# Performance work log

Measured on AMD Instinct MI355X. Metric: run time of the kernel, lower is better.

## Reference

```python
import jax, jax.numpy as jnp
import numpy as np

B, S, H, V = 64, 512, 1024, 32000


def setup_inputs() -> dict:
    key = jax.random.key(0)
    ks = jax.random.split(key, 20)
    sd = 0.02
    inp = {
        'x': jax.random.randint(ks[0], (B, 1), 0, V),
        'h_prev': jax.random.normal(ks[1], (B, H), dtype=jnp.float32),
        'annotations': jax.random.normal(ks[2], (B, S, H), dtype=jnp.float32),
        # embedding table
        'emb': jax.random.normal(ks[3], (V, H), dtype=jnp.float32) * sd,
        # attention MLP: Linear(2H -> H), ReLU, Linear(H -> 1)
        'attn_W1': jax.random.normal(ks[4], (H, 2 * H), dtype=jnp.float32) * sd,
        'attn_b1': jnp.zeros((H,), jnp.float32),
        'attn_W2': jax.random.normal(ks[5], (1, H), dtype=jnp.float32) * sd,
        'attn_b2': jnp.zeros((1,), jnp.float32),
        # GRU cell linears (input_size = 2H). NOTE: original code has a bug where
        # weights_hr is never used (r uses weights_hz); we replicate that, so no Whr.
        'W_ir': jax.random.normal(ks[6], (H, 2 * H), dtype=jnp.float32) * sd,
        'b_ir': jnp.zeros((H,), jnp.float32),
        'W_iz': jax.random.normal(ks[7], (H, 2 * H), dtype=jnp.float32) * sd,
        'b_iz': jnp.zeros((H,), jnp.float32),
        'W_in': jax.random.normal(ks[8], (H, 2 * H), dtype=jnp.float32) * sd,
        'b_in': jnp.zeros((H,), jnp.float32),
        'W_hz': jax.random.normal(ks[9], (H, H), dtype=jnp.float32) * sd,
        'b_hz': jnp.zeros((H,), jnp.float32),
        'W_hn': jax.random.normal(ks[10], (H, H), dtype=jnp.float32) * sd,
        'b_hn': jnp.zeros((H,), jnp.float32),
        # output projection H -> V
        'W_out': jax.random.normal(ks[11], (V, H), dtype=jnp.float32) * sd,
        'b_out': jnp.zeros((V,), jnp.float32),
    }
    return inp


def _lin(x, W, b):
    # torch nn.Linear: y = x @ W.T + b, W has shape (out, in)
    return x @ W.T + b


def reference(x, h_prev, annotations, emb, attn_W1, attn_b1, attn_W2, attn_b2,
              W_ir, b_ir, W_iz, b_iz, W_in, b_in, W_hz, b_hz, W_hn, b_hn,
              W_out, b_out):
    # embedding lookup, squeeze time dim: (B, H)
    embed = emb[x[:, 0]]

    # additive attention: concat(annotations, expanded hidden) -> MLP -> softmax
    # split W1 over the concat axis to avoid materializing the [B,S,2H] concat:
    # concat @ W1.T == annotations @ W1[:, :H].T + hidden @ W1[:, H:].T
    hA = jnp.einsum('bsh,kh->bsk', annotations, attn_W1[:, :H])  # (B,S,H)
    hB = h_prev @ attn_W1[:, H:].T                               # (B,H)
    hidden_act = jax.nn.relu(hA + hB[:, None, :] + attn_b1)
    scores = jnp.einsum('bsk,k->bs', hidden_act, attn_W2[0]) + attn_b2[0]
    attention_weights = jax.nn.softmax(scores, axis=1)[:, :, None]  # (B,S,1)

    # context vector
    context = jnp.sum(attention_weights * annotations, axis=1)  # (B,H)
    xc = jnp.concatenate([context, embed], axis=1)              # (B,2H)

    # GRU cell (faithful to the original, including the weights_hz reuse in r)
    hz = _lin(h_prev, W_hz, b_hz)
    z = jax.nn.sigmoid(_lin(xc, W_iz, b_iz) + hz)
    r = jax.nn.sigmoid(_lin(xc, W_ir, b_ir) + hz)  # bug replicated: uses W_hz
    g = jnp.tanh(_lin(xc, W_in, b_in) + r * _lin(h_prev, W_hn, b_hn))
    h_new = (1.0 - z) * g + z * h_prev

    output = _lin(h_new, W_out, b_out)  # (B,V)
    return output, h_new, attention_weights
```

## Files before the change

kernel.cpp:

```cpp
#include <hip/hip_runtime.h>


typedef __bf16 bf16;
typedef __attribute__((ext_vector_type(4))) float  f32x4;
typedef __attribute__((ext_vector_type(4))) float  fx4;
typedef __attribute__((ext_vector_type(8))) bf16   bf16x8;
typedef __attribute__((ext_vector_type(4))) bf16   bf16x4;
typedef __attribute__((ext_vector_type(4))) unsigned int u32x4;
typedef __attribute__((ext_vector_type(2))) unsigned int u32x2;

#define MFMA16x16x32(a, b, c) __builtin_amdgcn_mfma_f32_16x16x32_bf16(a, b, c, 0, 0, 0)

#define Bb   64
#define Ss   512
#define Hh   1024
#define Vv   32000
#define Mtot (Bb * Ss)

#define WS_HPREV_B   0
#define WS_HNEW_B    131072
#define WS_XC_B      262144
#define WS_W1A_B     524288
#define WS_P_HB      2621440
#define WS_P_HZ      3670016
#define WS_P_HN      4718592
#define WS_P_IZ      5767168
#define WS_P_IR      6815744
#define WS_P_IN      7864320
#define WS_SCORES    8912896
#define WS_CTX       11010048
#define WS_ANNB      13107200

#define OUT_LOGITS   0
#define OUT_HNEW     2048000
#define OUT_AW       2113536

__device__ __forceinline__ float bf2f(unsigned short u) {
    unsigned int x = ((unsigned int)u) << 16;
    float f;
    __builtin_memcpy(&f, &x, 4);
    return f;
}

__device__ __forceinline__ void gload_lds16(const bf16* g, bf16* l)
{
    __builtin_amdgcn_global_load_lds(
        (const __attribute__((address_space(1))) unsigned int*)g,
        (__attribute__((address_space(3))) unsigned int*)l,
        16, 0, 0);
}

__global__ void k_prep(const int* __restrict__ x, const float* __restrict__ h_prev,
                       const float* __restrict__ emb, const float* __restrict__ attn_W1,
                       bf16* __restrict__ h_prev_b, bf16* __restrict__ xc_b,
                       bf16* __restrict__ W1a_b)
{
    int bid = blockIdx.x, t = threadIdx.x;
    if (bid < 64) {
        int b = bid;
        int row = x[b];
        for (int i = t; i < Hh; i += 256) {
            h_prev_b[b * Hh + i]          = (bf16)h_prev[b * Hh + i];
            xc_b[b * 2048 + Hh + i]       = (bf16)emb[(size_t)row * Hh + i];
        }
    } else {
        int row = bid - 64;
        int k4 = t * 4;
        fx4 v = *(const fx4*)(attn_W1 + (size_t)row * 2048 + k4);
        bf16x4 o;
#pragma unroll
        for (int q = 0; q < 4; q++) o[q] = (bf16)v[q];
        *(bf16x4*)(W1a_b + (size_t)row * Hh + k4) = o;
    }
}

__global__ void k_convann(const float* __restrict__ ann, bf16* __restrict__ annb)
{
    size_t i = ((size_t)blockIdx.x * 256 + threadIdx.x) * 8;
    size_t stride = (size_t)gridDim.x * 256 * 8;
    size_t n = (size_t)Mtot * Hh;
    for (; i < n; i += stride) {
        fx4 v0 = *(const fx4*)(ann + i);
        fx4 v1 = *(const fx4*)(ann + i + 4);
        bf16x8 o;
#pragma unroll
        for (int q = 0; q < 4; q++) { o[q] = (bf16)v0[q]; o[q + 4] = (bf16)v1[q]; }
        *(bf16x8*)(annb + i) = o;
    }
}

__global__ __launch_bounds__(256, 2) void k_sgemm(
    const bf16* __restrict__ A, int lda, int kchunk,
    const float* __restrict__ B0, const float* __restrict__ B1, const float* __restrict__ B2,
    int ldb0, int ldb1, int ldb2,
    float* __restrict__ o0, float* __restrict__ o1, float* __restrict__ o2,
    const float* __restrict__ bias, int N, int finalOut)
{
    __shared__ __align__(16) bf16 lA[2][64][72];
    __shared__ __align__(16) bf16 lB[2][64][72];

    int nb = blockIdx.x, sk = blockIdx.y, mat = blockIdx.z;
    const float* Bp = (mat == 0) ? B0 : (mat == 1 ? B1 : B2);
    int ldb         = (mat == 0) ? ldb0 : (mat == 1 ? ldb1 : ldb2);
    float* op       = (mat == 0) ? o0 : (mat == 1 ? o1 : o2);

    int n0 = nb * 64, k0 = sk * kchunk;
    int t = threadIdx.x, lane = t & 63, wid = t >> 6;
    int srow = t >> 2, schunk = t & 3;

    const bf16*  agp = A  + (size_t)srow * lda + k0 + schunk * 16;
    const float* bgp = Bp + (size_t)(n0 + srow) * ldb + k0 + schunk * 16;

    f32x4 acc[4];
#pragma unroll
    for (int i = 0; i < 4; i++) acc[i] = (f32x4)0.0f;

    u32x4 aR0, aR1; fx4 bRf[4];
    int nk = kchunk >> 6;

    aR0 = *(const u32x4*)(agp);
    aR1 = *(const u32x4*)(agp + 8);
#pragma unroll
    for (int q = 0; q < 4; q++) bRf[q] = *(const fx4*)(bgp + q * 4);
    {
        *(u32x4*)&lA[0][srow][schunk * 16]     = aR0;
        *(u32x4*)&lA[0][srow][schunk * 16 + 8] = aR1;
        bf16x8 p0, p1;
#pragma unroll
        for (int q = 0; q < 4; q++) {
            p0[q] = (bf16)bRf[0][q]; p0[q + 4] = (bf16)bRf[1][q];
            p1[q] = (bf16)bRf[2][q]; p1[q + 4] = (bf16)bRf[3][q];
        }
        *(bf16x8*)&lB[0][srow][schunk * 16]     = p0;
        *(bf16x8*)&lB[0][srow][schunk * 16 + 8] = p1;
    }
    __syncthreads();

    int cur = 0;
    for (int ks = 0; ks < nk; ks++) {
        if (ks + 1 < nk) {
            aR0 = *(const u32x4*)(agp + (ks + 1) * 64);
            aR1 = *(const u32x4*)(agp + (ks + 1) * 64 + 8);
#pragma unroll
            for (int q = 0; q < 4; q++) bRf[q] = *(const fx4*)(bgp + (ks + 1) * 64 + q * 4);
        }
        int rA = lane & 15;
        int kc = (lane >> 4) * 8;
#pragma unroll
        for (int kk = 0; kk < 2; kk++) {
            bf16x8 bfr = *(bf16x8*)&lB[cur][wid * 16 + rA][kk * 32 + kc];
#pragma unroll
            for (int i = 0; i < 4; i++) {
                bf16x8 af = *(bf16x8*)&lA[cur][i * 16 + rA][kk * 32 + kc];
                acc[i] = MFMA16x16x32(af, bfr, acc[i]);
            }
        }
        if (ks + 1 < nk) {
            int nxt = cur ^ 1;
            *(u32x4*)&lA[nxt][srow][schunk * 16]     = aR0;
            *(u32x4*)&lA[nxt][srow][schunk * 16 + 8] = aR1;
            bf16x8 p0, p1;
#pragma unroll
            for (int q = 0; q < 4; q++) {
                p0[q] = (bf16)bRf[0][q]; p0[q + 4] = (bf16)bRf[1][q];
                p1[q] = (bf16)bRf[2][q]; p1[q + 4] = (bf16)bRf[3][q];
            }
            *(bf16x8*)&lB[nxt][srow][schunk * 16]     = p0;
            *(bf16x8*)&lB[nxt][srow][schunk * 16 + 8] = p1;
        }
        __syncthreads();
        cur ^= 1;
    }

    int n = n0 + wid * 16 + (lane & 15);
#pragma unroll
    for (int i = 0; i < 4; i++) {
#pragma unroll
        for (int r = 0; r < 4; r++) {
            int m = i * 16 + (lane >> 4) * 4 + r;
            float v = acc[i][r];
            if (finalOut) op[(size_t)m * N + n] = v + bias[n];
            else          op[(size_t)(sk * 64 + m) * N + n] = v;
        }
    }
}

__global__ __launch_bounds__(256, 4) void k_attn(
    const bf16* __restrict__ annb, const bf16* __restrict__ Bw,
    const float* __restrict__ p_hB, const float* __restrict__ b1,
    const float* __restrict__ W2, float* __restrict__ scores_part)
{
    __shared__ __align__(16) bf16 lA[2][4096];
    __shared__ __align__(16) bf16 lB[2][4096];

    int bid = blockIdx.x;
    int swz = (bid & 7) * 256 + (bid >> 3);
    int mb = swz >> 3, nb = swz & 7;

    int t = threadIdx.x, lane = t & 63, wid = t >> 6;
    int wm = wid >> 1, wn = wid & 1;

    int srow = t >> 2, sch = t & 3;
    int row1 = srow + 64;
    int g0 = (sch ^ ((srow >> 1) & 3)) << 3;
    int g1 = (sch ^ ((row1 >> 1) & 3)) << 3;
    const bf16* aS0 = annb + (size_t)(mb * 128 + srow) * 1024 + g0;
    const bf16* aS1 = annb + (size_t)(mb * 128 + row1) * 1024 + g1;
    const bf16* bS0 = Bw   + (size_t)(nb * 128 + srow) * 1024 + g0;
    const bf16* bS1 = Bw   + (size_t)(nb * 128 + row1) * 1024 + g1;
    int lo0 = wid * 512;
    int lo1 = 2048 + wid * 512;

#define STAGE(buf, kt) do { \
        gload_lds16(aS0 + (size_t)(kt) * 32, &lA[buf][lo0]); \
        gload_lds16(aS1 + (size_t)(kt) * 32, &lA[buf][lo1]); \
        gload_lds16(bS0 + (size_t)(kt) * 32, &lB[buf][lo0]); \
        gload_lds16(bS1 + (size_t)(kt) * 32, &lB[buf][lo1]); \
    } while (0)

    f32x4 acc[4][4];
#pragma unroll
    for (int i = 0; i < 4; i++)
#pragma unroll
        for (int j = 0; j < 4; j++) acc[i][j] = (f32x4)0.0f;

    STAGE(0, 0);
    __syncthreads();

    int r = lane & 15, q = lane >> 4;
    int cur = 0;
    for (int kt = 0; kt < 32; kt++) {
        if (kt < 31) STAGE(cur ^ 1, kt + 1);

        bf16x8 af[4], bfr[4];
#pragma unroll
        for (int i = 0; i < 4; i++) {
            int rA = wm * 64 + i * 16 + r;
            af[i] = *(const bf16x8*)&lA[cur][rA * 32 + ((q ^ ((rA >> 1) & 3)) << 3)];
        }
#pragma unroll
        for (int j = 0; j < 4; j++) {
            int rB = wn * 64 + j * 16 + r;
            bfr[j] = *(const bf16x8*)&lB[cur][rB * 32 + ((q ^ ((rB >> 1) & 3)) << 3)];
        }
#pragma unroll
        for (int i = 0; i < 4; i++)
#pragma unroll
            for (int j = 0; j < 4; j++)
                acc[i][j] = MFMA16x16x32(af[i], bfr[j], acc[i][j]);

        __syncthreads();
        cur ^= 1;
    }
#undef STAGE

    int m0 = mb * 128, n0 = nb * 128;
    int b = m0 >> 9;
    float hb[4], w2v[4];
#pragma unroll
    for (int j = 0; j < 4; j++) {
        int n = n0 + wn * 64 + j * 16 + r;
        float h = p_hB[b * Hh + n] + p_hB[65536 + b * Hh + n]
                + p_hB[131072 + b * Hh + n] + p_hB[196608 + b * Hh + n];
        hb[j]  = h + b1[n];
        w2v[j] = W2[n];
    }
    float red[16];
#pragma unroll
    for (int i = 0; i < 4; i++)
#pragma unroll
        for (int rr = 0; rr < 4; rr++) {
            float s = 0.f;
#pragma unroll
            for (int j = 0; j < 4; j++) {
                float v = acc[i][j][rr] + hb[j];
                v = fmaxf(v, 0.f);
                s += v * w2v[j];
            }
            red[i * 4 + rr] = s;
        }
#pragma unroll
    for (int mask = 1; mask <= 8; mask <<= 1)
#pragma unroll
        for (int p = 0; p < 16; p++)
            red[p] += __shfl_xor(red[p], mask, 64);

    if (r == 0) {
        float* sp = scores_part + (size_t)(nb * 2 + wn) * Mtot + m0 + wm * 64 + q * 4;
#pragma unroll
        for (int i = 0; i < 4; i++)
#pragma unroll
            for (int rr = 0; rr < 4; rr++)
                sp[i * 16 + rr] = red[i * 4 + rr];
    }
}

__global__ void k_softmax(const float* __restrict__ scores_part, float* __restrict__ aw)
{
    int b = blockIdx.x, s = threadIdx.x;
    int lane = s & 63, wid = s >> 6;
    float v = 0.f;
#pragma unroll
    for (int p = 0; p < 16; p++) v += scores_part[(size_t)p * Mtot + b * Ss + s];

    __shared__ float redm[8], redsum[8];
    float m = v;
#pragma unroll
    for (int mask = 32; mask; mask >>= 1) m = fmaxf(m, __shfl_xor(m, mask, 64));
    if (lane == 0) redm[wid] = m;
    __syncthreads();
    float bm = redm[0];
#pragma unroll
    for (int w = 1; w < 8; w++) bm = fmaxf(bm, redm[w]);

    float e = expf(v - bm);
    float ss = e;
#pragma unroll
    for (int mask = 32; mask; mask >>= 1) ss += __shfl_xor(ss, mask, 64);
    if (lane == 0) redsum[wid] = ss;
    __syncthreads();
    float tot = 0.f;
#pragma unroll
    for (int w = 0; w < 8; w++) tot += redsum[w];

    aw[b * Ss + s] = e / tot;
}

__global__ void k_context(const bf16* __restrict__ annb, const float* __restrict__ aw,
                          float* __restrict__ ctx_part)
{
    __shared__ float law[64];
    int bid = blockIdx.x;
    int b = bid >> 3, sc = bid & 7;
    int t = threadIdx.x;
    if (t < 64) law[t] = aw[b * Ss + sc * 64 + t];
    __syncthreads();
    int h0 = t * 4;
    const bf16* ap = annb + (size_t)(b * Ss + sc * 64) * Hh + h0;
    float a0 = 0, a1 = 0, a2 = 0, a3 = 0;
#pragma unroll 4
    for (int s2 = 0; s2 < 64; s2++) {
        float w = law[s2];
        u32x2 v = *(const u32x2*)(ap + (size_t)s2 * Hh);
        a0 += w * bf2f((unsigned short)(v[0] & 0xffff));
        a1 += w * bf2f((unsigned short)(v[0] >> 16));
        a2 += w * bf2f((unsigned short)(v[1] & 0xffff));
        a3 += w * bf2f((unsigned short)(v[1] >> 16));
    }
    fx4 o; o[0] = a0; o[1] = a1; o[2] = a2; o[3] = a3;
    *(fx4*)(ctx_part + sc * 65536 + b * Hh + h0) = o;
}

__global__ void k_xc(const float* __restrict__ ctx_part, bf16* __restrict__ xc_b)
{
    int idx = blockIdx.x * 256 + threadIdx.x;
    float c = 0.f;
#pragma unroll
    for (int p = 0; p < 8; p++) c += ctx_part[p * 65536 + idx];
    int b = idx >> 10, h = idx & 1023;
    xc_b[b * 2048 + h] = (bf16)c;
}

__global__ void k_gru(const float* __restrict__ p_iz, const float* __restrict__ p_ir,
                      const float* __restrict__ p_in, const float* __restrict__ p_hz,
                      const float* __restrict__ p_hn,
                      const float* __restrict__ b_iz, const float* __restrict__ b_ir,
                      const float* __restrict__ b_in, const float* __restrict__ b_hz,
                      const float* __restrict__ b_hn,
                      const float* __restrict__ h_prev,
                      float* __restrict__ out_h, bf16* __restrict__ h_new_b)
{
    int idx = blockIdx.x * 256 + threadIdx.x;
    int o = idx & 1023;
    float iz = p_iz[idx] + p_iz[65536 + idx] + p_iz[131072 + idx] + p_iz[196608 + idx];
    float ir = p_ir[idx] + p_ir[65536 + idx] + p_ir[131072 + idx] + p_ir[196608 + idx];
    float in_ = p_in[idx] + p_in[65536 + idx] + p_in[131072 + idx] + p_in[196608 + idx];
    float hz = p_hz[idx] + p_hz[65536 + idx] + p_hz[131072 + idx] + p_hz[196608 + idx];
    float hn = p_hn[idx] + p_hn[65536 + idx] + p_hn[131072 + idx] + p_hn[196608 + idx];
    hz += b_hz[o];
    hn += b_hn[o];
    float z = 1.f / (1.f + expf(-(iz + b_iz[o] + hz)));
    float r = 1.f / (1.f + expf(-(ir + b_ir[o] + hz)));
    float g = tanhf(in_ + b_in[o] + r * hn);
    float hp = h_prev[idx];
    float hnew = (1.f - z) * g + z * hp;
    out_h[idx] = hnew;
    h_new_b[idx] = (bf16)hnew;
}

extern "C" void kernel_launch(void* const* d_in, const int* in_sizes, int n_in,
                              void* d_out, int out_size, void* d_ws, size_t ws_size,
                              hipStream_t stream)
{
    const int*   x        = (const int*)d_in[0];
    const float* h_prev   = (const float*)d_in[1];
    const float* ann      = (const float*)d_in[2];
    const float* emb      = (const float*)d_in[3];
    const float* attn_W1  = (const float*)d_in[4];
    const float* attn_b1  = (const float*)d_in[5];
    const float* attn_W2  = (const float*)d_in[6];
    const float* W_ir     = (const float*)d_in[8];
    const float* b_ir     = (const float*)d_in[9];
    const float* W_iz     = (const float*)d_in[10];
    const float* b_iz     = (const float*)d_in[11];
    const float* W_in     = (const float*)d_in[12];
    const float* b_in     = (const float*)d_in[13];
    const float* W_hz     = (const float*)d_in[14];
    const float* b_hz     = (const float*)d_in[15];
    const float* W_hn     = (const float*)d_in[16];
    const float* b_hn     = (const float*)d_in[17];
    const float* W_out    = (const float*)d_in[18];
    const float* b_out    = (const float*)d_in[19];

    float* out = (float*)d_out;
    char*  ws  = (char*)d_ws;

    bf16*  h_prev_b = (bf16*)(ws + WS_HPREV_B);
    bf16*  h_new_b  = (bf16*)(ws + WS_HNEW_B);
    bf16*  xc_b     = (bf16*)(ws + WS_XC_B);
    bf16*  W1a_b    = (bf16*)(ws + WS_W1A_B);
    float* p_hB     = (float*)(ws + WS_P_HB);
    float* p_hz     = (float*)(ws + WS_P_HZ);
    float* p_hn     = (float*)(ws + WS_P_HN);
    float* p_iz     = (float*)(ws + WS_P_IZ);
    float* p_ir     = (float*)(ws + WS_P_IR);
    float* p_in     = (float*)(ws + WS_P_IN);
    float* scores_p = (float*)(ws + WS_SCORES);
    float* ctx_part = (float*)(ws + WS_CTX);
    bf16*  annb     = (bf16*)(ws + WS_ANNB);

    k_prep<<<1088, 256, 0, stream>>>(x, h_prev, emb, attn_W1, h_prev_b, xc_b, W1a_b);
    k_convann<<<2048, 256, 0, stream>>>(ann, annb);

    {
        dim3 g(16, 4, 3);
        k_sgemm<<<g, 256, 0, stream>>>(h_prev_b, 1024, 256,
                                       attn_W1 + 1024, W_hz, W_hn, 2048, 1024, 1024,
                                       p_hB, p_hz, p_hn, nullptr, 1024, 0);
    }

    k_attn<<<2048, 256, 0, stream>>>(annb, W1a_b, p_hB, attn_b1, attn_W2, scores_p);

    k_softmax<<<64, 512, 0, stream>>>(scores_p, out + OUT_AW);

    k_context<<<512, 256, 0, stream>>>(annb, out + OUT_AW, ctx_part);

    k_xc<<<256, 256, 0, stream>>>(ctx_part, xc_b);

    {
        dim3 g(16, 4, 3);
        k_sgemm<<<g, 256, 0, stream>>>(xc_b, 2048, 512,
                                       W_iz, W_ir, W_in, 2048, 2048, 2048,
                                       p_iz, p_ir, p_in, nullptr, 1024, 0);
    }

    k_gru<<<256, 256, 0, stream>>>(p_iz, p_ir, p_in, p_hz, p_hn,
                                   b_iz, b_ir, b_in, b_hz, b_hn,
                                   h_prev, out + OUT_HNEW, h_new_b);

    {
        dim3 g(500, 1, 1);
        k_sgemm<<<g, 256, 0, stream>>>(h_new_b, 1024, 1024,
                                       W_out, W_out, W_out, 1024, 1024, 1024,
                                       out + OUT_LOGITS, nullptr, nullptr,
                                       b_out, 32000, 1);
    }
}
```

Measured before the change: 186.0 us.

## Rewrite attention GEMM with 256x256 tiles and phased LDS pipeline

The attention-score GEMM moves from 128x128 tiles with 4 waves to 256x256 tiles with 8 waves and K=64 steps. Tiles are staged in 128KB of dynamic shared memory, double-buffered in half-tile pieces and interleaved across four compute phases, using explicit vmcnt waits, barriers and s_setprio around the MFMA bursts. The goal is more data reuse per global load and better overlap of loads with MFMA work. In exchange, register pressure rises (32 accumulators per wave), only one workgroup fits per CU, and correctness now depends on a hand-tuned wait and barrier schedule.

Result: faster. 173.6 us (-6.7%).

```diff
diff --git a/kernel.cpp b/kernel.cpp
--- a/kernel.cpp
+++ b/kernel.cpp
@@ -185,89 +185,127 @@
     }
 }
 
-__global__ __launch_bounds__(256, 4) void k_attn(
+__global__ __launch_bounds__(512, 2) void k_attn(
     const bf16* __restrict__ annb, const bf16* __restrict__ Bw,
     const float* __restrict__ p_hB, const float* __restrict__ b1,
     const float* __restrict__ W2, float* __restrict__ scores_part)
 {
-    __shared__ __align__(16) bf16 lA[2][4096];
-    __shared__ __align__(16) bf16 lB[2][4096];
+    extern __shared__ char smem[];
 
     int bid = blockIdx.x;
-    int swz = (bid & 7) * 256 + (bid >> 3);
-    int mb = swz >> 3, nb = swz & 7;
+    int wgid = (bid & 7) * 64 + (bid >> 3);
+    int mb = wgid >> 2, nbp = wgid & 3;
 
     int t = threadIdx.x, lane = t & 63, wid = t >> 6;
-    int wm = wid >> 1, wn = wid & 1;
-
-    int srow = t >> 2, sch = t & 3;
-    int row1 = srow + 64;
-    int g0 = (sch ^ ((srow >> 1) & 3)) << 3;
-    int g1 = (sch ^ ((row1 >> 1) & 3)) << 3;
-    const bf16* aS0 = annb + (size_t)(mb * 128 + srow) * 1024 + g0;
-    const bf16* aS1 = annb + (size_t)(mb * 128 + row1) * 1024 + g1;
-    const bf16* bS0 = Bw   + (size_t)(nb * 128 + srow) * 1024 + g0;
-    const bf16* bS1 = Bw   + (size_t)(nb * 128 + row1) * 1024 + g1;
-    int lo0 = wid * 512;
-    int lo1 = 2048 + wid * 512;
-
-#define STAGE(buf, kt) do { \
-        gload_lds16(aS0 + (size_t)(kt) * 32, &lA[buf][lo0]); \
-        gload_lds16(aS1 + (size_t)(kt) * 32, &lA[buf][lo1]); \
-        gload_lds16(bS0 + (size_t)(kt) * 32, &lB[buf][lo0]); \
-        gload_lds16(bS1 + (size_t)(kt) * 32, &lB[buf][lo1]); \
+    int wm = wid >> 2, wn = wid & 3;
+    int r = lane & 15, q = lane >> 4;
+
+    int srow = t >> 3;
+    int gc   = (t & 7) ^ (srow & 7);
+    size_t goff = (size_t)srow * 1024 + gc * 8;
+    int doff = wid * 1024;
+
+    const bf16* aSrc = annb + (size_t)mb * 262144;
+    const bf16* bSrc = Bw   + (size_t)nbp * 262144;
+
+    int rowAoff = (wm * 64 + r) * 128;
+    int rowBoff = (wn * 32 + r) * 128;
+    int e0 = (q ^ (r & 7)) * 16;
+    int e1 = e0 ^ 64;
+
+#define STAGEOP(src, half, buf, mat, kt) do {                                  \
+        const bf16* s_ = (src) + (half) * 131072 + (size_t)(kt) * 64 + goff;   \
+        char* d_ = smem + (buf) * 65536 + (mat) * 32768 + (half) * 16384 + doff; \
+        gload_lds16(s_, (bf16*)d_);                                            \
+        gload_lds16(s_ + 65536, (bf16*)(d_ + 8192));                           \
     } while (0)
 
-    f32x4 acc[4][4];
-#pragma unroll
-    for (int i = 0; i < 4; i++)
+#define VM4 asm volatile("s_waitcnt vmcnt(4)" ::: "memory")
+#define VM0 asm volatile("s_waitcnt vmcnt(0)" ::: "memory")
+
+    f32x4 acc[8][4];
+#pragma unroll
+    for (int i = 0; i < 8; i++)
 #pragma unroll
         for (int j = 0; j < 4; j++) acc[i][j] = (f32x4)0.0f;
 
-    STAGE(0, 0);
-    __syncthreads();
-
-    int r = lane & 15, q = lane >> 4;
-    int cur = 0;
-    for (int kt = 0; kt < 32; kt++) {
-        if (kt < 31) STAGE(cur ^ 1, kt + 1);
-
-        bf16x8 af[4], bfr[4];
-#pragma unroll
-        for (int i = 0; i < 4; i++) {
-            int rA = wm * 64 + i * 16 + r;
-            af[i] = *(const bf16x8*)&lA[cur][rA * 32 + ((q ^ ((rA >> 1) & 3)) << 3)];
-        }
-#pragma unroll
-        for (int j = 0; j < 4; j++) {
-            int rB = wn * 64 + j * 16 + r;
-            bfr[j] = *(const bf16x8*)&lB[cur][rB * 32 + ((q ^ ((rB >> 1) & 3)) << 3)];
-        }
-#pragma unroll
-        for (int i = 0; i < 4; i++)
-#pragma unroll
-            for (int j = 0; j < 4; j++)
-                acc[i][j] = MFMA16x16x32(af[i], bfr[j], acc[i][j]);
-
-        __syncthreads();
-        cur ^= 1;
-    }
-#undef STAGE
-
-    int m0 = mb * 128, n0 = nb * 128;
+    bf16x8 bq[4];
+
+#define PH(AH, KS, READB, STG, ENDW) do {                                      \
+        const char* pa_ = smem + cur * 65536 + (AH) * 16384 + rowAoff;         \
+        bf16x8 aq[4];                                                          \
+        _Pragma("unroll")                                                      \
+        for (int ip = 0; ip < 4; ip++)                                         \
+            aq[ip] = *(const bf16x8*)(pa_ + ip * 2048 + ((KS) ? e1 : e0));     \
+        if (READB) {                                                           \
+            _Pragma("unroll")                                                  \
+            for (int jp = 0; jp < 4; jp++) {                                   \
+                const char* pb_ = smem + cur * 65536 + 32768                   \
+                                + (jp >> 1) * 16384 + rowBoff;                 \
+                bq[jp] = *(const bf16x8*)(pb_ + (jp & 1) * 2048 + ((KS) ? e1 : e0)); \
+            }                                                                  \
+        }                                                                      \
+        STG;                                                                   \
+        __builtin_amdgcn_s_barrier();                                          \
+        __builtin_amdgcn_s_setprio(1);                                         \
+        _Pragma("unroll")                                                      \
+        for (int ip = 0; ip < 4; ip++)                                         \
+            _Pragma("unroll")                                                  \
+            for (int jp = 0; jp < 4; jp++)                                     \
+                acc[(AH) * 4 + ip][jp] =                                       \
+                    MFMA16x16x32(aq[ip], bq[jp], acc[(AH) * 4 + ip][jp]);      \
+        __builtin_amdgcn_s_setprio(0);                                         \
+        ENDW;                                                                  \
+        __builtin_amdgcn_s_barrier();                                          \
+    } while (0)
+
+#define TILE(tt, S1, S2, VMW)                                                  \
+        PH(0, 0, 1, if (S1) STAGEOP(aSrc, 1, nxt, 0, (tt) + 1), );             \
+        PH(1, 0, 0, if (S1) STAGEOP(bSrc, 1, nxt, 1, (tt) + 1), );             \
+        PH(0, 1, 1, , );                                                       \
+        PH(1, 1, 0, if (S2) { STAGEOP(aSrc, 0, cur, 0, (tt) + 2);              \
+                              STAGEOP(bSrc, 0, cur, 1, (tt) + 2); }, VMW);
+
+    STAGEOP(aSrc, 0, 0, 0, 0);
+    STAGEOP(bSrc, 0, 0, 1, 0);
+    STAGEOP(aSrc, 1, 0, 0, 0);
+    STAGEOP(bSrc, 1, 0, 1, 0);
+    STAGEOP(aSrc, 0, 1, 0, 1);
+    STAGEOP(bSrc, 0, 1, 1, 1);
+    VM4;
+    __builtin_amdgcn_s_barrier();
+
+#pragma unroll 1
+    for (int kt = 0; kt < 14; kt++) {
+        int cur = kt & 1, nxt = cur ^ 1;
+        TILE(kt, 1, 1, VM4);
+    }
+    {
+        int cur = 0, nxt = 1;
+        TILE(14, 1, 0, VM0);
+    }
+    {
+        int cur = 1, nxt = 0;
+        TILE(15, 0, 0, );
+    }
+#undef TILE
+#undef PH
+#undef STAGEOP
+
+    int m0 = mb * 256, n0g = nbp * 256;
     int b = m0 >> 9;
     float hb[4], w2v[4];
 #pragma unroll
     for (int j = 0; j < 4; j++) {
-        int n = n0 + wn * 64 + j * 16 + r;
+        int n = n0g + (j >> 1) * 128 + wn * 32 + (j & 1) * 16 + r;
         float h = p_hB[b * Hh + n] + p_hB[65536 + b * Hh + n]
                 + p_hB[131072 + b * Hh + n] + p_hB[196608 + b * Hh + n];
         hb[j]  = h + b1[n];
         w2v[j] = W2[n];
     }
-    float red[16];
-#pragma unroll
-    for (int i = 0; i < 4; i++)
+    float red[32];
+#pragma unroll
+    for (int i = 0; i < 8; i++)
 #pragma unroll
         for (int rr = 0; rr < 4; rr++) {
             float s = 0.f;
@@ -282,16 +320,18 @@
 #pragma unroll
     for (int mask = 1; mask <= 8; mask <<= 1)
 #pragma unroll
-        for (int p = 0; p < 16; p++)
+        for (int p = 0; p < 32; p++)
             red[p] += __shfl_xor(red[p], mask, 64);
 
     if (r == 0) {
-        float* sp = scores_part + (size_t)(nb * 2 + wn) * Mtot + m0 + wm * 64 + q * 4;
-#pragma unroll
-        for (int i = 0; i < 4; i++)
+        float* sp = scores_part + (size_t)(nbp * 4 + wn) * Mtot;
+#pragma unroll
+        for (int i = 0; i < 8; i++) {
+            int m = m0 + wm * 64 + (i & 3) * 16 + (i >> 2) * 128 + q * 4;
 #pragma unroll
             for (int rr = 0; rr < 4; rr++)
-                sp[i * 16 + rr] = red[i * 4 + rr];
+                sp[m + rr] = red[i * 4 + rr];
+        }
     }
 }
 
@@ -429,6 +469,9 @@
     float* ctx_part = (float*)(ws + WS_CTX);
     bf16*  annb     = (bf16*)(ws + WS_ANNB);
 
+    hipFuncSetAttribute(reinterpret_cast<const void*>(k_attn),
+                        hipFuncAttributeMaxDynamicSharedMemorySize, 131072);
+
     k_prep<<<1088, 256, 0, stream>>>(x, h_prev, emb, attn_W1, h_prev_b, xc_b, W1a_b);
     k_convann<<<2048, 256, 0, stream>>>(ann, annb);
 
@@ -439,7 +482,7 @@
                                        p_hB, p_hz, p_hn, nullptr, 1024, 0);
     }
 
-    k_attn<<<2048, 256, 0, stream>>>(annb, W1a_b, p_hB, attn_b1, attn_W2, scores_p);
+    k_attn<<<512, 512, 131072, stream>>>(annb, W1a_b, p_hB, attn_b1, attn_W2, scores_p);
 
     k_softmax<<<64, 512, 0, stream>>>(scores_p, out + OUT_AW);
 
```

## Fuse prep kernels and retile attention GEMM to 256x256 with 4-stage LDS pipeline

Applied to the files above, without the earlier changes.

Merges the embedding/W1 conversion, the annotation fp32-to-bf16 conversion and the h_prev GEMMs into one kernel. That kernel converts h_prev and weights inline, so the separate h_prev bf16 buffer and two launches go away. The attention-score GEMM moves from 128x128 tiles with 256 threads and double buffering to 256x256 tiles with 512 threads. It uses a 4-deep global-to-LDS prefetch ring (128 KB dynamic LDS), explicit vmcnt waits, raw barriers and MFMA priority boosting, aiming to raise operand reuse and hide load latency. The trade-off is one block per CU from the large LDS footprint, higher register pressure with 32 accumulators per lane, and a fused kernel that mixes heterogeneous block roles.

Result: faster. 169.2 us (-9.0%).

```diff
diff --git a/kernel.cpp b/kernel.cpp
--- a/kernel.cpp
+++ b/kernel.cpp
@@ -17,7 +17,6 @@
 #define Vv   32000
 #define Mtot (Bb * Ss)
 
-#define WS_HPREV_B   0
 #define WS_HNEW_B    131072
 #define WS_XC_B      262144
 #define WS_W1A_B     524288
@@ -50,43 +49,134 @@
         16, 0, 0);
 }
 
-__global__ void k_prep(const int* __restrict__ x, const float* __restrict__ h_prev,
-                       const float* __restrict__ emb, const float* __restrict__ attn_W1,
-                       bf16* __restrict__ h_prev_b, bf16* __restrict__ xc_b,
-                       bf16* __restrict__ W1a_b)
-{
+__global__ __launch_bounds__(256, 2) void k_pre(
+    const int* __restrict__ x, const float* __restrict__ h_prev,
+    const float* __restrict__ emb, const float* __restrict__ attn_W1,
+    const float* __restrict__ W_hz, const float* __restrict__ W_hn,
+    const float* __restrict__ ann,
+    bf16* __restrict__ xc_b, bf16* __restrict__ W1a_b, bf16* __restrict__ annb,
+    float* __restrict__ p_hB, float* __restrict__ p_hz, float* __restrict__ p_hn)
+{
+    __shared__ __align__(16) bf16 lA[2][64][72];
+    __shared__ __align__(16) bf16 lB[2][64][72];
+
     int bid = blockIdx.x, t = threadIdx.x;
-    if (bid < 64) {
-        int b = bid;
-        int row = x[b];
-        for (int i = t; i < Hh; i += 256) {
-            h_prev_b[b * Hh + i]          = (bf16)h_prev[b * Hh + i];
-            xc_b[b * 2048 + Hh + i]       = (bf16)emb[(size_t)row * Hh + i];
-        }
-    } else {
-        int row = bid - 64;
-        int k4 = t * 4;
-        fx4 v = *(const fx4*)(attn_W1 + (size_t)row * 2048 + k4);
-        bf16x4 o;
-#pragma unroll
-        for (int q = 0; q < 4; q++) o[q] = (bf16)v[q];
-        *(bf16x4*)(W1a_b + (size_t)row * Hh + k4) = o;
-    }
-}
-
-__global__ void k_convann(const float* __restrict__ ann, bf16* __restrict__ annb)
-{
-    size_t i = ((size_t)blockIdx.x * 256 + threadIdx.x) * 8;
-    size_t stride = (size_t)gridDim.x * 256 * 8;
-    size_t n = (size_t)Mtot * Hh;
-    for (; i < n; i += stride) {
-        fx4 v0 = *(const fx4*)(ann + i);
-        fx4 v1 = *(const fx4*)(ann + i + 4);
-        bf16x8 o;
-#pragma unroll
-        for (int q = 0; q < 4; q++) { o[q] = (bf16)v0[q]; o[q + 4] = (bf16)v1[q]; }
-        *(bf16x8*)(annb + i) = o;
-    }
+
+    if (bid >= 1280) {
+        size_t i = ((size_t)(bid - 1280) * 256 + t) * 8;
+        size_t stride = (size_t)2048 * 256 * 8;
+        size_t n = (size_t)Mtot * Hh;
+        for (; i < n; i += stride) {
+            fx4 v0 = *(const fx4*)(ann + i);
+            fx4 v1 = *(const fx4*)(ann + i + 4);
+            bf16x8 o;
+#pragma unroll
+            for (int q = 0; q < 4; q++) { o[q] = (bf16)v0[q]; o[q + 4] = (bf16)v1[q]; }
+            *(bf16x8*)(annb + i) = o;
+        }
+        return;
+    }
+    if (bid >= 192) {
+        int sub = bid - 192;
+        if (sub < 64) {
+            int b = sub, row = x[b];
+            for (int i = t; i < Hh; i += 256)
+                xc_b[b * 2048 + Hh + i] = (bf16)emb[(size_t)row * Hh + i];
+        } else {
+            int row = sub - 64;
+            int k4 = t * 4;
+            fx4 v = *(const fx4*)(attn_W1 + (size_t)row * 2048 + k4);
+            bf16x4 o;
+#pragma unroll
+            for (int q = 0; q < 4; q++) o[q] = (bf16)v[q];
+            *(bf16x4*)(W1a_b + (size_t)row * Hh + k4) = o;
+        }
+        return;
+    }
+
+    int nb = bid & 15, sk = (bid >> 4) & 3, mat = bid >> 6;
+    const float* Bp = (mat == 0) ? (attn_W1 + 1024) : (mat == 1 ? W_hz : W_hn);
+    int ldb         = (mat == 0) ? 2048 : 1024;
+    float* op       = (mat == 0) ? p_hB : (mat == 1 ? p_hz : p_hn);
+
+    int n0 = nb * 64, k0 = sk * 256;
+    int lane = t & 63, wid = t >> 6;
+    int srow = t >> 2, schunk = t & 3;
+
+    const float* agp = h_prev + (size_t)srow * 1024 + k0 + schunk * 16;
+    const float* bgp = Bp + (size_t)(n0 + srow) * ldb + k0 + schunk * 16;
+
+    f32x4 acc[4];
+#pragma unroll
+    for (int i = 0; i < 4; i++) acc[i] = (f32x4)0.0f;
+
+    fx4 aRf[4], bRf[4];
+#pragma unroll
+    for (int q = 0; q < 4; q++) { aRf[q] = *(const fx4*)(agp + q * 4);
+                                  bRf[q] = *(const fx4*)(bgp + q * 4); }
+    {
+        bf16x8 a0, a1, p0, p1;
+#pragma unroll
+        for (int q = 0; q < 4; q++) {
+            a0[q] = (bf16)aRf[0][q]; a0[q + 4] = (bf16)aRf[1][q];
+            a1[q] = (bf16)aRf[2][q]; a1[q + 4] = (bf16)aRf[3][q];
+            p0[q] = (bf16)bRf[0][q]; p0[q + 4] = (bf16)bRf[1][q];
+            p1[q] = (bf16)bRf[2][q]; p1[q + 4] = (bf16)bRf[3][q];
+        }
+        *(bf16x8*)&lA[0][srow][schunk * 16]     = a0;
+        *(bf16x8*)&lA[0][srow][schunk * 16 + 8] = a1;
+        *(bf16x8*)&lB[0][srow][schunk * 16]     = p0;
+        *(bf16x8*)&lB[0][srow][schunk * 16 + 8] = p1;
+    }
+    __syncthreads();
+
+    int cur = 0;
+    for (int ks = 0; ks < 4; ks++) {
+        if (ks + 1 < 4) {
+#pragma unroll
+            for (int q = 0; q < 4; q++) {
+                aRf[q] = *(const fx4*)(agp + (ks + 1) * 64 + q * 4);
+                bRf[q] = *(const fx4*)(bgp + (ks + 1) * 64 + q * 4);
+            }
+        }
+        int rA = lane & 15;
+        int kc = (lane >> 4) * 8;
+#pragma unroll
+        for (int kk = 0; kk < 2; kk++) {
+            bf16x8 bfr = *(bf16x8*)&lB[cur][wid * 16 + rA][kk * 32 + kc];
+#pragma unroll
+            for (int i = 0; i < 4; i++) {
+                bf16x8 af = *(bf16x8*)&lA[cur][i * 16 + rA][kk * 32 + kc];
+                acc[i] = MFMA16x16x32(af, bfr, acc[i]);
+            }
+        }
+        if (ks + 1 < 4) {
+            int nxt = cur ^ 1;
+            bf16x8 a0, a1, p0, p1;
+#pragma unroll
+            for (int q = 0; q < 4; q++) {
+                a0[q] = (bf16)aRf[0][q]; a0[q + 4] = (bf16)aRf[1][q];
+                a1[q] = (bf16)aRf[2][q]; a1[q + 4] = (bf16)aRf[3][q];
+                p0[q] = (bf16)bRf[0][q]; p0[q + 4] = (bf16)bRf[1][q];
+                p1[q] = (bf16)bRf[2][q]; p1[q + 4] = (bf16)bRf[3][q];
+            }
+            *(bf16x8*)&lA[nxt][srow][schunk * 16]     = a0;
+            *(bf16x8*)&lA[nxt][srow][schunk * 16 + 8] = a1;
+            *(bf16x8*)&lB[nxt][srow][schunk * 16]     = p0;
+            *(bf16x8*)&lB[nxt][srow][schunk * 16 + 8] = p1;
+        }
+        __syncthreads();
+        cur ^= 1;
+    }
+
+    int n = n0 + wid * 16 + (lane & 15);
+#pragma unroll
+    for (int i = 0; i < 4; i++)
+#pragma unroll
+        for (int r = 0; r < 4; r++) {
+            int m = i * 16 + (lane >> 4) * 4 + r;
+            op[(size_t)(sk * 64 + m) * 1024 + n] = acc[i][r];
+        }
 }
 
 __global__ __launch_bounds__(256, 2) void k_sgemm(
@@ -185,89 +275,93 @@
     }
 }
 
-__global__ __launch_bounds__(256, 4) void k_attn(
+__global__ __launch_bounds__(512, 2) void k_attn(
     const bf16* __restrict__ annb, const bf16* __restrict__ Bw,
     const float* __restrict__ p_hB, const float* __restrict__ b1,
     const float* __restrict__ W2, float* __restrict__ scores_part)
 {
-    __shared__ __align__(16) bf16 lA[2][4096];
-    __shared__ __align__(16) bf16 lB[2][4096];
+    extern __shared__ char smem[];
 
     int bid = blockIdx.x;
-    int swz = (bid & 7) * 256 + (bid >> 3);
-    int mb = swz >> 3, nb = swz & 7;
+    int wgid = (bid & 7) * 64 + (bid >> 3);
+    int mb = wgid >> 2, nbp = wgid & 3;
 
     int t = threadIdx.x, lane = t & 63, wid = t >> 6;
-    int wm = wid >> 1, wn = wid & 1;
-
-    int srow = t >> 2, sch = t & 3;
-    int row1 = srow + 64;
-    int g0 = (sch ^ ((srow >> 1) & 3)) << 3;
-    int g1 = (sch ^ ((row1 >> 1) & 3)) << 3;
-    const bf16* aS0 = annb + (size_t)(mb * 128 + srow) * 1024 + g0;
-    const bf16* aS1 = annb + (size_t)(mb * 128 + row1) * 1024 + g1;
-    const bf16* bS0 = Bw   + (size_t)(nb * 128 + srow) * 1024 + g0;
-    const bf16* bS1 = Bw   + (size_t)(nb * 128 + row1) * 1024 + g1;
-    int lo0 = wid * 512;
-    int lo1 = 2048 + wid * 512;
-
-#define STAGE(buf, kt) do { \
-        gload_lds16(aS0 + (size_t)(kt) * 32, &lA[buf][lo0]); \
-        gload_lds16(aS1 + (size_t)(kt) * 32, &lA[buf][lo1]); \
-        gload_lds16(bS0 + (size_t)(kt) * 32, &lB[buf][lo0]); \
-        gload_lds16(bS1 + (size_t)(kt) * 32, &lB[buf][lo1]); \
+    int wm = wid >> 2, wn = wid & 3;
+    int r = lane & 15, q = lane >> 4;
+
+    const bf16* aS = annb + (size_t)mb  * 262144
+                   + (size_t)(wid * 32 + (lane >> 2)) * 1024 + (lane & 3) * 8;
+    const bf16* bS = Bw   + (size_t)nbp * 262144
+                   + (size_t)(wid * 32 + (lane >> 2)) * 1024 + (lane & 3) * 8;
+    int sld = wid * 2048;
+
+#define STAGE(kt) do { int bq_ = ((kt) & 3) * 32768;                         \
+        const bf16* a_ = aS + (kt) * 32;                                     \
+        const bf16* b_ = bS + (kt) * 32;                                     \
+        gload_lds16(a_,         (bf16*)(smem + bq_ + sld));                  \
+        gload_lds16(a_ + 16384, (bf16*)(smem + bq_ + sld + 1024));           \
+        gload_lds16(b_,         (bf16*)(smem + bq_ + 16384 + sld));          \
+        gload_lds16(b_ + 16384, (bf16*)(smem + bq_ + 16384 + sld + 1024));   \
     } while (0)
 
-    f32x4 acc[4][4];
-#pragma unroll
-    for (int i = 0; i < 4; i++)
+    int rAo[8], rBo[4];
+#pragma unroll
+    for (int i = 0; i < 8; i++)
+        rAo[i] = (wm * 64 + (i & 3) * 16 + (i >> 2) * 128 + r) * 64 + q * 16;
+#pragma unroll
+    for (int j = 0; j < 4; j++)
+        rBo[j] = 16384 + (wn * 32 + (j & 1) * 16 + (j >> 1) * 128 + r) * 64 + q * 16;
+
+    f32x4 acc[8][4];
+#pragma unroll
+    for (int i = 0; i < 8; i++)
 #pragma unroll
         for (int j = 0; j < 4; j++) acc[i][j] = (f32x4)0.0f;
 
-    STAGE(0, 0);
-    __syncthreads();
-
-    int r = lane & 15, q = lane >> 4;
-    int cur = 0;
+    STAGE(0); STAGE(1); STAGE(2);
+    asm volatile("s_waitcnt vmcnt(8)" ::: "memory");
+    __builtin_amdgcn_s_barrier();
+
+#pragma unroll 1
     for (int kt = 0; kt < 32; kt++) {
-        if (kt < 31) STAGE(cur ^ 1, kt + 1);
-
-        bf16x8 af[4], bfr[4];
-#pragma unroll
-        for (int i = 0; i < 4; i++) {
-            int rA = wm * 64 + i * 16 + r;
-            af[i] = *(const bf16x8*)&lA[cur][rA * 32 + ((q ^ ((rA >> 1) & 3)) << 3)];
-        }
-#pragma unroll
-        for (int j = 0; j < 4; j++) {
-            int rB = wn * 64 + j * 16 + r;
-            bfr[j] = *(const bf16x8*)&lB[cur][rB * 32 + ((q ^ ((rB >> 1) & 3)) << 3)];
-        }
-#pragma unroll
-        for (int i = 0; i < 4; i++)
+        const char* base = smem + (kt & 3) * 32768;
+        bf16x8 aq[8], bq[4];
+#pragma unroll
+        for (int i = 0; i < 8; i++) aq[i] = *(const bf16x8*)(base + rAo[i]);
+#pragma unroll
+        for (int j = 0; j < 4; j++) bq[j] = *(const bf16x8*)(base + rBo[j]);
+        if (kt < 29) STAGE(kt + 3);
+
+        __builtin_amdgcn_s_setprio(1);
+#pragma unroll
+        for (int i = 0; i < 8; i++)
 #pragma unroll
             for (int j = 0; j < 4; j++)
-                acc[i][j] = MFMA16x16x32(af[i], bfr[j], acc[i][j]);
-
-        __syncthreads();
-        cur ^= 1;
+                acc[i][j] = MFMA16x16x32(aq[i], bq[j], acc[i][j]);
+        __builtin_amdgcn_s_setprio(0);
+
+        if (kt < 29)       { asm volatile("s_waitcnt vmcnt(8)" ::: "memory"); }
+        else if (kt == 29) { asm volatile("s_waitcnt vmcnt(4)" ::: "memory"); }
+        else if (kt == 30) { asm volatile("s_waitcnt vmcnt(0)" ::: "memory"); }
+        if (kt < 31) __builtin_amdgcn_s_barrier();
     }
 #undef STAGE
 
-    int m0 = mb * 128, n0 = nb * 128;
+    int m0 = mb * 256, n0g = nbp * 256;
     int b = m0 >> 9;
     float hb[4], w2v[4];
 #pragma unroll
     for (int j = 0; j < 4; j++) {
-        int n = n0 + wn * 64 + j * 16 + r;
+        int n = n0g + (j >> 1) * 128 + wn * 32 + (j & 1) * 16 + r;
         float h = p_hB[b * Hh + n] + p_hB[65536 + b * Hh + n]
                 + p_hB[131072 + b * Hh + n] + p_hB[196608 + b * Hh + n];
         hb[j]  = h + b1[n];
         w2v[j] = W2[n];
     }
-    float red[16];
-#pragma unroll
-    for (int i = 0; i < 4; i++)
+    float red[32];
+#pragma unroll
+    for (int i = 0; i < 8; i++)
 #pragma unroll
         for (int rr = 0; rr < 4; rr++) {
             float s = 0.f;
@@ -282,16 +376,18 @@
 #pragma unroll
     for (int mask = 1; mask <= 8; mask <<= 1)
 #pragma unroll
-        for (int p = 0; p < 16; p++)
+        for (int p = 0; p < 32; p++)
             red[p] += __shfl_xor(red[p], mask, 64);
 
     if (r == 0) {
-        float* sp = scores_part + (size_t)(nb * 2 + wn) * Mtot + m0 + wm * 64 + q * 4;
-#pragma unroll
-        for (int i = 0; i < 4; i++)
+        float* sp = scores_part + (size_t)(nbp * 4 + wn) * Mtot;
+#pragma unroll
+        for (int i = 0; i < 8; i++) {
+            int m = m0 + wm * 64 + (i & 3) * 16 + (i >> 2) * 128 + q * 4;
 #pragma unroll
             for (int rr = 0; rr < 4; rr++)
-                sp[i * 16 + rr] = red[i * 4 + rr];
+                sp[m + rr] = red[i * 4 + rr];
+        }
     }
 }
 
@@ -415,7 +511,6 @@
     float* out = (float*)d_out;
     char*  ws  = (char*)d_ws;
 
-    bf16*  h_prev_b = (bf16*)(ws + WS_HPREV_B);
     bf16*  h_new_b  = (bf16*)(ws + WS_HNEW_B);
     bf16*  xc_b     = (bf16*)(ws + WS_XC_B);
     bf16*  W1a_b    = (bf16*)(ws + WS_W1A_B);
@@ -429,17 +524,14 @@
     float* ctx_part = (float*)(ws + WS_CTX);
     bf16*  annb     = (bf16*)(ws + WS_ANNB);
 
-    k_prep<<<1088, 256, 0, stream>>>(x, h_prev, emb, attn_W1, h_prev_b, xc_b, W1a_b);
-    k_convann<<<2048, 256, 0, stream>>>(ann, annb);
-
-    {
-        dim3 g(16, 4, 3);
-        k_sgemm<<<g, 256, 0, stream>>>(h_prev_b, 1024, 256,
-                                       attn_W1 + 1024, W_hz, W_hn, 2048, 1024, 1024,
-                                       p_hB, p_hz, p_hn, nullptr, 1024, 0);
-    }
-
-    k_attn<<<2048, 256, 0, stream>>>(annb, W1a_b, p_hB, attn_b1, attn_W2, scores_p);
+    hipFuncSetAttribute(reinterpret_cast<const void*>(k_attn),
+                        hipFuncAttributeMaxDynamicSharedMemorySize, 131072);
+
+    k_pre<<<3328, 256, 0, stream>>>(x, h_prev, emb, attn_W1, W_hz, W_hn, ann,
+                                    xc_b, W1a_b, annb, p_hB, p_hz, p_hn);
+
+    k_attn<<<512, 512, 131072, stream>>>(annb, W1a_b, p_hB, attn_b1, attn_W2,
+                                         scores_p);
 
     k_softmax<<<64, 512, 0, stream>>>(scores_p, out + OUT_AW);
 
```
